# Optimization experiments

Measured on AMD Instinct MI355X. Metric: run time of the kernel, lower is better.

Reference implementation:

```python
import jax, jax.numpy as jnp
import numpy as np

S, B, C, H, W = 5, 2, 128, 24, 24
N_ITER = 3
BN_EPS = 1e-5


def conv2d(x, w, b, pad):
    # x: (N, Cin, H, W), w: (Cout, Cin, kh, kw)
    y = jax.lax.conv_general_dilated(
        x, w, (1, 1), [(pad, pad), (pad, pad)],
        dimension_numbers=('NCHW', 'OIHW', 'NCHW'))
    return y + b[None, :, None, None]


def setup_inputs() -> dict:
    key = jax.random.key(0)
    ks = jax.random.split(key, 8)
    sc = 0.03  # keep pre-softmax logits in a sane range
    d = {}
    d['x'] = jax.random.normal(ks[0], (S, B, C, H, W), jnp.float32) * 0.5
    d['Wf_w'] = jax.random.normal(ks[1], (C, C, 3, 3), jnp.float32) * sc
    d['Wf_b'] = jnp.zeros((C,), jnp.float32)
    d['Wh_w'] = jax.random.normal(ks[2], (C, C, 3, 3), jnp.float32) * sc
    d['Wh_b'] = jnp.zeros((C,), jnp.float32)
    d['Wl_w'] = jax.random.normal(ks[3], (C, C, 3, 3), jnp.float32) * sc
    d['Wl_b'] = jnp.zeros((C,), jnp.float32)
    d['alpha'] = jnp.ones((1,), jnp.float32)
    d['Wc'] = jax.random.normal(ks[4], (C, C), jnp.float32) * sc
    d['Wg_w'] = jax.random.normal(ks[5], (C, C, 3, 3), jnp.float32) * sc
    d['Wg_b'] = jnp.zeros((C,), jnp.float32)
    d['bn_gamma'] = jnp.ones((C,), jnp.float32)
    d['bn_beta'] = jnp.zeros((C,), jnp.float32)
    d['gru_zr_w'] = jax.random.normal(ks[6], (2 * C, 2 * C, 5, 5), jnp.float32) * sc
    d['gru_zr_b'] = jnp.zeros((2 * C,), jnp.float32)
    d['gru_h_w'] = jax.random.normal(ks[7], (C, 2 * C, 5, 5), jnp.float32) * sc
    d['gru_h_b'] = jnp.zeros((C,), jnp.float32)
    d['intra_w'] = jnp.full((1,), 0.5, jnp.float32)
    d['inter_w'] = jnp.full((1,), 0.5, jnp.float32)
    return d


def reference(x, Wf_w, Wf_b, Wh_w, Wh_b, Wl_w, Wl_b, alpha, Wc, Wg_w, Wg_b,
              bn_gamma, bn_beta, gru_zr_w, gru_zr_b, gru_h_w, gru_h_b,
              intra_w, inter_w):
    S_, B_, C_, H_, W_ = x.shape
    N = H_ * W_
    # BatchNorm2d in inference mode with fresh running stats (mean=0, var=1)
    bn_scale = bn_gamma / jnp.sqrt(1.0 + BN_EPS)
    mask = (1.0 - jnp.eye(S_, dtype=x.dtype))[:, :, None, None, None, None]
    h = x
    for _ in range(N_ITER):
        hb = h.reshape(S_ * B_, C_, H_, W_)
        # ---- intra-node self-attention (per node in sequence) ----
        ft = conv2d(hb, Wf_w, Wf_b, 1).reshape(S_, B_, C_, N)
        ht = conv2d(hb, Wh_w, Wh_b, 1).reshape(S_, B_, C_, N)
        lt = conv2d(hb, Wl_w, Wl_b, 1).reshape(S_, B_, C_, N)
        att = jax.nn.softmax(jnp.einsum('sbcn,sbcm->sbnm', ft, ht), axis=-1)
        ctx = jnp.einsum('sbnm,sbcm->sbcn', att, lt).reshape(S_, B_, C_, H_, W_)
        eii = alpha[0] * ctx + h
        # ---- inter-node pairwise attention messages (all i,j pairs) ----
        hf = h.reshape(S_, B_, C_, N)
        yt = jnp.einsum('cd,jbdn->jbcn', Wc, hf)
        eij = jnp.einsum('ibcn,jbcm->ijbnm', hf, yt)  # (S,S,B,N,N)
        eijn = jax.nn.softmax(eij, axis=-1)
        mji = jnp.einsum('ijbnm,jbcm->ijbcn', eijn, hf)  # (S,S,B,C,N)
        m4 = mji.reshape(S_ * S_ * B_, C_, H_, W_)
        g = jax.nn.sigmoid(jnp.mean(conv2d(m4, Wg_w, Wg_b, 1),
                                    axis=(2, 3), keepdims=True))
        mg = (g * m4) * bn_scale[None, :, None, None] + bn_beta[None, :, None, None]
        mg = mg.reshape(S_, S_, B_, C_, H_, W_)
        inter = jnp.sum(mg * mask, axis=1)  # exclude j == i
        msg = intra_w[0] * eii + inter_w[0] * inter
        # ---- ConvGRU update + residual ----
        xi = msg.reshape(S_ * B_, C_, H_, W_)
        zr = jax.nn.sigmoid(conv2d(jnp.concatenate([xi, hb], axis=1),
                                   gru_zr_w, gru_zr_b, 2))
        z, r = zr[:, :C_], zr[:, C_:]
        h_hat = jnp.tanh(conv2d(jnp.concatenate([xi, r * hb], axis=1),
                                gru_h_w, gru_h_b, 2))
        h_new = (1.0 - z) * hb + z * h_hat
        h = (h_new + hb).reshape(S_, B_, C_, H_, W_)
    return h
```

## Files before the change

### kernel.cpp

```cpp
#include <hip/hip_runtime.h>
#include <math.h>

#define S_  5
#define B_  2
#define C_  128
#define N_  576
#define SB  10
#define NPAIR 40
#define C2  256

typedef short v8s __attribute__((ext_vector_type(8)));
typedef float v4f __attribute__((ext_vector_type(4)));

#define GLOBAL_AS __attribute__((address_space(1)))
#define LDS_AS    __attribute__((address_space(3)))

__device__ __forceinline__ unsigned short f2bf(float f) {
    union { float f; unsigned u; } v; v.f = f;
    unsigned r = (v.u + 0x7FFF + ((v.u >> 16) & 1)) >> 16;
    return (unsigned short)r;
}
__device__ __forceinline__ float bf2f(unsigned short h) {
    union { unsigned u; float f; } v; v.u = ((unsigned)h) << 16;
    return v.f;
}

__device__ __forceinline__ void packA5_body(int idx, const float* __restrict__ w,
                                            unsigned short* __restrict__ Apk, int M)
{
    if (idx >= M * 6400) return;
    int r = idx;
    int j = r & 7;      r >>= 3;
    int quad = r & 3;   r >>= 2;
    int l15 = r & 15;   r >>= 4;
    int c = r & 3;      r >>= 2;
    int tap_l = r % 5;  r /= 5;
    int g = r % 5;      r /= 5;
    int ch = r & 1;     r >>= 1;
    int kk = r & 3;     r >>= 2;
    int cgb = r;
    int co = cgb * 64 + c * 16 + l15;
    int ci = kk * 64 + ch * 32 + quad * 8 + j;
    int tap = g * 5 + tap_l;
    Apk[idx] = f2bf(w[((size_t)co * 256 + ci) * 25 + tap]);
}
__device__ __forceinline__ void packA3_body(int idx, const float* __restrict__ wf,
                                            const float* __restrict__ wh,
                                            const float* __restrict__ wl,
                                            unsigned short* __restrict__ Apk)
{
    if (idx >= 384 * 1152) return;
    int r = idx;
    int j = r & 7;      r >>= 3;
    int quad = r & 3;   r >>= 2;
    int l15 = r & 15;   r >>= 4;
    int c = r & 3;      r >>= 2;
    int tap_l = r % 3;  r /= 3;
    int g = r % 3;      r /= 3;
    int ch = r & 1;     r >>= 1;
    int kk = r & 1;     r >>= 1;
    int cgb = r;
    int co = cgb * 64 + c * 16 + l15;
    const float* w = (co < 128) ? wf : (co < 256) ? wh : wl;
    int cl = co & 127;
    int ci = kk * 64 + ch * 32 + quad * 8 + j;
    int tap = g * 3 + tap_l;
    Apk[idx] = f2bf(w[((size_t)cl * 128 + ci) * 9 + tap]);
}
__device__ __forceinline__ void packWc_body(int idx, const float* __restrict__ w,
                                            unsigned short* __restrict__ o)
{
    if (idx < 128 * 128) o[idx] = f2bf(w[idx]);
}
__device__ __forceinline__ void packWgT_body(int idx, const float* __restrict__ w,
                                             float* __restrict__ o)
{
    if (idx >= 128 * 1152) return;
    int co = idx & 127, i = idx >> 7;
    o[(size_t)i * 128 + co] = w[(size_t)co * 1152 + i];
}

__device__ __forceinline__ void tc_body(
    int px0, int img,
    const float* __restrict__ src, const float* __restrict__ zrp,
    const float* __restrict__ zrb,
    unsigned short* __restrict__ dst, unsigned short* __restrict__ vfd)
{
    const size_t PLANE = (size_t)SB * C2 * N_;
    __shared__ float tile[128][9];
    int t = threadIdx.x;
    #pragma unroll
    for (int i = 0; i < 4; ++i) {
        int e = i * 256 + t; int ci = e >> 3; int px = e & 7;
        float v = src[((size_t)img * 128 + ci) * 576 + px0 + px];
        if (zrp) {
            size_t zi = ((size_t)img * C2 + 128 + ci) * 576 + px0 + px;
            float a = zrb[128 + ci];
            #pragma unroll
            for (int k = 0; k < 4; ++k) a += zrp[k * PLANE + zi];
            v *= 1.f / (1.f + __expf(-a));
        }
        tile[ci][px] = v;
        if (vfd) {
            int m = px0 + px;
            int ctile = ci >> 4, l15v = ci & 15;
            int sIdx = m >> 5, quadv = (m >> 3) & 3, j = m & 7;
            vfd[(((size_t)img * 8 + ctile) * 18 + sIdx) * 512 + (quadv * 16 + l15v) * 8 + j] = f2bf(v);
        }
    }
    __syncthreads();
    #pragma unroll
    for (int i = 0; i < 4; ++i) {
        int e = i * 256 + t; int pxl = e >> 7; int ci = e & 127;
        dst[((size_t)img * 576 + px0 + pxl) * 128 + ci] = f2bf(tile[ci][pxl]);
    }
}

__global__ __launch_bounds__(256) void tc_kernel(
    const float* __restrict__ src, const float* __restrict__ zrp,
    const float* __restrict__ zrb,
    unsigned short* __restrict__ dst, unsigned short* __restrict__ vfd)
{
    tc_body(blockIdx.x * 8, blockIdx.y, src, zrp, zrb, dst, vfd);
}

#define NB_A3   1728
#define NB_A5ZR 6400
#define NB_A5H  3200
#define NB_WC   64
#define NB_WGT  576
#define NB_TC   720
__global__ __launch_bounds__(256) void pack_all_kernel(
    const float* __restrict__ Wf_w, const float* __restrict__ Wh_w,
    const float* __restrict__ Wl_w, unsigned short* __restrict__ Wp3,
    const float* __restrict__ zr_w, unsigned short* __restrict__ Wpzr,
    const float* __restrict__ gh_w, unsigned short* __restrict__ Wph,
    const float* __restrict__ Wc,  unsigned short* __restrict__ Wcb,
    const float* __restrict__ Wg_w, float* __restrict__ WgT,
    const float* __restrict__ x, unsigned short* __restrict__ hT16,
    unsigned short* __restrict__ VFi)
{
    int bid = blockIdx.x, t = threadIdx.x;
    if (bid < NB_A3) {
        packA3_body(bid * 256 + t, Wf_w, Wh_w, Wl_w, Wp3);
    } else if (bid < NB_A3 + NB_A5ZR) {
        packA5_body((bid - NB_A3) * 256 + t, zr_w, Wpzr, 256);
    } else if (bid < NB_A3 + NB_A5ZR + NB_A5H) {
        packA5_body((bid - NB_A3 - NB_A5ZR) * 256 + t, gh_w, Wph, 128);
    } else if (bid < NB_A3 + NB_A5ZR + NB_A5H + NB_WC) {
        packWc_body((bid - NB_A3 - NB_A5ZR - NB_A5H) * 256 + t, Wc, Wcb);
    } else if (bid < NB_A3 + NB_A5ZR + NB_A5H + NB_WC + NB_WGT) {
        packWgT_body((bid - NB_A3 - NB_A5ZR - NB_A5H - NB_WC) * 256 + t, Wg_w, WgT);
    } else {
        int b2 = bid - (NB_A3 + NB_A5ZR + NB_A5H + NB_WC + NB_WGT);
        tc_body((b2 % 72) * 8, b2 / 72, x, nullptr, nullptr, hT16, VFi);
    }
}

template<int KD, int R, int CINT, int SPLITK, int MODE>
__device__ __forceinline__ void conv_body(
    int bx, int by, int bz,
    const unsigned short* __restrict__ srcA, const unsigned short* __restrict__ srcB,
    const unsigned short* __restrict__ Apk, int COUT, float* __restrict__ po,
    const float* __restrict__ b0, const float* __restrict__ b1, const float* __restrict__ b2,
    unsigned short* __restrict__ t0, unsigned short* __restrict__ t1,
    unsigned short* __restrict__ t2)
{
    constexpr int PART   = CINT / SPLITK;
    constexpr int NCH    = PART / 32;
    constexpr int NSUB   = NCH * KD;
    constexpr int WR     = 8 + 2 * R;
    constexpr int WC     = 24 + 2 * R;
    constexpr int NPOS   = WR * WC;
    constexpr int NSLOTB = NPOS * 4;
    constexpr int RB     = (NSLOTB + 255) / 256;
    constexpr int AUNITS = KD * 4 * 64;
    constexpr int AR     = AUNITS / 256;
    __shared__ __align__(16) unsigned short Ab[2][AUNITS * 8];
    __shared__ __align__(16) unsigned short Bb[NPOS * 32];

    int f   = bx;
    int kk  = f % SPLITK;
    int cgb = f / SPLITK;
    int pxb = by;
    int img = bz;
    int t = threadIdx.x;
    int wave = t >> 6, lane = t & 63;
    int quad = lane >> 4, l15 = lane & 15;
    int r0 = pxb * 8;

    const int cibase = kk * PART;
    const unsigned short* src = (cibase >= 128) ? srcB : srcA;
    const int cioff0 = cibase & 127;
    const unsigned short* srcI = src + (size_t)img * 576 * 128;

    int posBase[3], pxs[3];
    #pragma unroll
    for (int s = 0; s < 3; ++s) {
        int px = pxb * 192 + wave * 48 + s * 16 + l15;
        pxs[s] = px;
        int pr = px / 24, pc = px % 24;
        posBase[s] = (pr - r0 + R) * WC + pc + R;
    }

    int goffB[RB]; bool gokB[RB];
    #pragma unroll
    for (int rr = 0; rr < RB; ++rr) {
        int idx = rr * 256 + wave * 64 + lane;
        int pos = idx >> 2, slotq = idx & 3;
        int gr = slotq ^ ((pos >> 1) & 3);
        int wr = pos / WC, wc = pos % WC;
        int grow = r0 - R + wr, gcol = wc - R;
        gokB[rr] = (idx < NSLOTB) && grow >= 0 && grow < 24 && gcol >= 0 && gcol < 24;
        goffB[rr] = (grow * 24 + gcol) * 128 + gr * 8;
    }

    auto stageB = [&](int ch) {
        const unsigned short* sp = srcI + cioff0 + ch * 32;
        #pragma unroll
        for (int rr = 0; rr < RB; ++rr) {
            if (gokB[rr]) {
                __builtin_amdgcn_global_load_lds(
                    (const GLOBAL_AS void*)(sp + goffB[rr]),
                    (LDS_AS void*)((char*)&Bb[0] + (size_t)(rr * 256 + wave * 64) * 16),
                    16, 0, 0);
            }
        }
    };
    auto stageA = [&](int sub, int buf) {
        const unsigned short* sp = Apk + ((size_t)((cgb * SPLITK + kk) * NSUB + sub)) * (AUNITS * 8);
        #pragma unroll
        for (int r = 0; r < AR; ++r) {
            int u0 = r * 256 + wave * 64;
            __builtin_amdgcn_global_load_lds(
                (const GLOBAL_AS void*)(sp + (size_t)(u0 + lane) * 8),
                (LDS_AS void*)((char*)&Ab[buf][0] + (size_t)u0 * 16),
                16, 0, 0);
        }
    };

    v4f acc[4][3];
    #pragma unroll
    for (int c = 0; c < 4; ++c)
        #pragma unroll
        for (int s = 0; s < 3; ++s)
            #pragma unroll
            for (int r = 0; r < 4; ++r) acc[c][s][r] = 0.f;

    {
        v8s zv;
        #pragma unroll
        for (int j = 0; j < 8; ++j) zv[j] = 0;
        for (int i = t; i < NPOS * 4; i += 256) ((v8s*)Bb)[i] = zv;
    }
    __syncthreads();
    stageB(0);
    stageA(0, 0);
    __syncthreads();

    int sub = 0;
    #pragma unroll 1
    for (int ch = 0; ch < NCH; ++ch) {
        #pragma unroll 1
        for (int g = 0; g < KD; ++g) {
            if (sub + 1 < NSUB) stageA(sub + 1, (sub + 1) & 1);
            const unsigned short* Ap = &Ab[sub & 1][0];
            #pragma unroll
            for (int tl = 0; tl < KD; ++tl) {
                int doff = (g - R) * WC + (tl - R);
                v8s a[4];
                #pragma unroll
                for (int c = 0; c < 4; ++c)
                    a[c] = *(const v8s*)&Ap[((tl * 4 + c) * 64 + l15 * 4 + quad) * 8];
                v8s b[3];
                #pragma unroll
                for (int s = 0; s < 3; ++s) {
                    int pos = posBase[s] + doff;
                    b[s] = *(const v8s*)&Bb[pos * 32 + ((quad ^ ((pos >> 1) & 3)) << 3)];
                }
                #pragma unroll
                for (int c = 0; c < 4; ++c)
                    #pragma unroll
                    for (int s = 0; s < 3; ++s)
                        acc[c][s] = __builtin_amdgcn_mfma_f32_16x16x32_bf16(a[c], b[s], acc[c][s], 0, 0, 0);
            }
            __syncthreads();
            ++sub;
        }
        if (ch + 1 < NCH) { stageB(ch + 1); __syncthreads(); }
    }

    if (MODE == 0) {
        float* out = po + (size_t)kk * ((size_t)SB * COUT * 576)
                   + ((size_t)img * COUT + cgb * 64) * 576;
        #pragma unroll
        for (int c = 0; c < 4; ++c)
            #pragma unroll
            for (int s = 0; s < 3; ++s)
                #pragma unroll
                for (int r = 0; r < 4; ++r) {
                    int col = c * 16 + quad * 4 + r;
                    out[(size_t)col * 576 + pxs[s]] = acc[c][s][r];
                }
    } else {
        #pragma unroll
        for (int c = 0; c < 4; ++c)
            #pragma unroll
            for (int s = 0; s < 3; ++s) {
                int px = pxs[s];
                #pragma unroll
                for (int r = 0; r < 4; ++r) {
                    int co = cgb * 64 + c * 16 + quad * 4 + r;
                    int which = co >> 7, cl = co & 127;
                    const float* bp = (which == 0) ? b0 : (which == 1) ? b1 : b2;
                    float v = acc[c][s][r] + bp[cl];
                    if (which == 0) {
                        t0[((size_t)img * 576 + px) * 128 + cl] = f2bf(v);
                    } else if (which == 1) {
                        int mt = px >> 4, l15m = px & 15;
                        int kb = cl >> 5, quadk = (cl >> 3) & 3, jj = cl & 7;
                        t1[(((size_t)img * 36 + mt) * 4 + kb) * 512 + (quadk * 16 + l15m) * 8 + jj] = f2bf(v);
                    } else {
                        int ctile = cl >> 4, l15v = cl & 15;
                        int sIdx = px >> 5, quadv = (px >> 3) & 3, jj = px & 7;
                        t2[(((size_t)img * 8 + ctile) * 18 + sIdx) * 512 + (quadv * 16 + l15v) * 8 + jj] = f2bf(v);
                    }
                }
            }
    }
}

template<int KD, int R, int CINT, int SPLITK, int MODE>
__global__ __launch_bounds__(256, 1) void conv_mfma(
    const unsigned short* __restrict__ srcA, const unsigned short* __restrict__ srcB,
    const unsigned short* __restrict__ Apk, int COUT, float* __restrict__ po,
    const float* __restrict__ b0, const float* __restrict__ b1, const float* __restrict__ b2,
    unsigned short* __restrict__ t0, unsigned short* __restrict__ t1,
    unsigned short* __restrict__ t2)
{
    conv_body<KD, R, CINT, SPLITK, MODE>(blockIdx.x, blockIdx.y, blockIdx.z,
        srcA, srcB, Apk, COUT, po, b0, b1, b2, t0, t1, t2);
}

__device__ __forceinline__ void yt_body(
    int mt, int img,
    const unsigned short* __restrict__ hT, const unsigned short* __restrict__ Wcb,
    unsigned short* __restrict__ KFi)
{
    int t = threadIdx.x, wave = t >> 6, lane = t & 63;
    int q = lane >> 4, l15 = lane & 15;
    int n0 = mt * 16;
    v4f acc[2];
    #pragma unroll
    for (int ct = 0; ct < 2; ++ct)
        #pragma unroll
        for (int r = 0; r < 4; ++r) acc[ct][r] = 0.f;
    #pragma unroll
    for (int kk = 0; kk < 4; ++kk) {
        v8s b = *(const v8s*)(hT + ((size_t)img * 576 + n0 + l15) * 128 + kk * 32 + q * 8);
        #pragma unroll
        for (int ct = 0; ct < 2; ++ct) {
            v8s a = *(const v8s*)(Wcb + (size_t)((wave * 2 + ct) * 16 + l15) * 128 + kk * 32 + q * 8);
            acc[ct] = __builtin_amdgcn_mfma_f32_16x16x32_bf16(a, b, acc[ct], 0, 0, 0);
        }
    }
    #pragma unroll
    for (int ct = 0; ct < 2; ++ct) {
        #pragma unroll
        for (int r = 0; r < 4; ++r) {
            int co = (wave * 2 + ct) * 16 + q * 4 + r;
            int kk = co >> 5, quadk = (co >> 3) & 3, j = co & 7;
            KFi[(((size_t)img * 36 + mt) * 4 + kk) * 512 + (quadk * 16 + l15) * 8 + j]
                = f2bf(acc[ct][r]);
        }
    }
}

__global__ __launch_bounds__(256, 1) void conv3_yt_kernel(
    const unsigned short* __restrict__ hT, const unsigned short* __restrict__ Wp3,
    const float* __restrict__ Wf_b, const float* __restrict__ Wh_b,
    const float* __restrict__ Wl_b,
    unsigned short* __restrict__ ftT, unsigned short* __restrict__ KFa,
    unsigned short* __restrict__ VFa,
    const unsigned short* __restrict__ Wcb, unsigned short* __restrict__ KFi)
{
    int bid = blockIdx.x;
    if (bid < 180) {
        conv_body<3, 1, 128, 1, 1>(bid % 6, (bid / 6) % 3, bid / 18,
            hT, hT, Wp3, 384, nullptr, Wf_b, Wh_b, Wl_b, ftT, KFa, VFa);
    } else {
        int b2 = bid - 180;
        yt_body(b2 % 36, b2 / 36, hT, Wcb, KFi);
    }
}

__global__ __launch_bounds__(256) void attn_merged(
    const unsigned short* __restrict__ QTi, const unsigned short* __restrict__ KFa,
    const unsigned short* __restrict__ VFa, float* __restrict__ Of,
    const float* __restrict__ addsrc, const float* __restrict__ alpha,
    const unsigned short* __restrict__ QTe, const unsigned short* __restrict__ KFe,
    const unsigned short* __restrict__ VFe, unsigned short* __restrict__ Oh,
    float* __restrict__ wpart)
{
    __shared__ __align__(16) unsigned short P[32 * 576];
    __shared__ float redmx[4][32];
    __shared__ float redsm[4][32];
    int t = threadIdx.x;
    int wave = t >> 6, lane = t & 63;
    int q = lane >> 4, l15 = lane & 15;

    int bid = blockIdx.x;
    int xcd = bid & 7, slot = bid >> 3;
    int gs = (xcd < 4) ? xcd * 113 + slot : 452 + (xcd - 4) * 112 + slot;
    int p = gs / 18;
    int mt2 = gs - p * 18;
    int n0 = mt2 * 32;

    bool intra = (p < SB);
    int pp = 0;
    const unsigned short *Qp, *Kp, *Vp;
    if (intra) {
        Qp = QTi + ((size_t)p * 576 + n0) * 128;
        Kp = KFa + (size_t)p * 36 * 4 * 512;
        Vp = VFa + (size_t)p * 8 * 18 * 512;
    } else {
        int pe = p - SB;
        int j = pe >> 3; int t2 = pe & 7;
        int b = t2 & 1;  int ii = t2 >> 1;
        int i = ii + (ii >= j ? 1 : 0);
        int qimg = i * 2 + b, kimg = j * 2 + b;
        pp = (i * 4 + (j - (j > i ? 1 : 0))) * 2 + b;
        Qp = QTe + ((size_t)qimg * 576 + n0) * 128;
        Kp = KFe + (size_t)kimg * 36 * 4 * 512;
        Vp = VFe + (size_t)kimg * 8 * 18 * 512;
    }

    v8s aq[2][4];
    #pragma unroll
    for (int qt = 0; qt < 2; ++qt)
        #pragma unroll
        for (int kk = 0; kk < 4; ++kk)
            aq[qt][kk] = *(const v8s*)(Qp + (size_t)(qt * 16 + l15) * 128 + kk * 32 + q * 8);

    v4f S[2][9];
    #pragma unroll
    for (int qt = 0; qt < 2; ++qt)
        #pragma unroll
        for (int i = 0; i < 9; ++i)
            #pragma unroll
            for (int r = 0; r < 4; ++r) S[qt][i][r] = 0.f;

    #pragma unroll
    for (int i = 0; i < 9; ++i) {
        int mtk = wave * 9 + i;
        #pragma unroll
        for (int kk = 0; kk < 4; ++kk) {
            v8s b = *(const v8s*)(Kp + ((size_t)(mtk * 4 + kk)) * 512 + lane * 8);
            S[0][i] = __builtin_amdgcn_mfma_f32_16x16x32_bf16(aq[0][kk], b, S[0][i], 0, 0, 0);
            S[1][i] = __builtin_amdgcn_mfma_f32_16x16x32_bf16(aq[1][kk], b, S[1][i], 0, 0, 0);
        }
    }

    #pragma unroll
    for (int qt = 0; qt < 2; ++qt) {
        #pragma unroll
        for (int r = 0; r < 4; ++r) {
            float m = S[qt][0][r];
            #pragma unroll
            for (int i = 1; i < 9; ++i) m = fmaxf(m, S[qt][i][r]);
            #pragma unroll
            for (int off = 1; off < 16; off <<= 1) m = fmaxf(m, __shfl_xor(m, off));
            if (l15 == 0) redmx[wave][qt * 16 + q * 4 + r] = m;
        }
    }
    __syncthreads();
    float sum[2][4];
    #pragma unroll
    for (int qt = 0; qt < 2; ++qt) {
        #pragma unroll
        for (int r = 0; r < 4; ++r) {
            int rr = qt * 16 + q * 4 + r;
            float g = fmaxf(fmaxf(redmx[0][rr], redmx[1][rr]),
                            fmaxf(redmx[2][rr], redmx[3][rr]));
            float s = 0.f;
            #pragma unroll
            for (int i = 0; i < 9; ++i) { float e = __expf(S[qt][i][r] - g); S[qt][i][r] = e; s += e; }
            #pragma unroll
            for (int off = 1; off < 16; off <<= 1) s += __shfl_xor(s, off);
            sum[qt][r] = s;
        }
    }
    if (l15 == 0) {
        #pragma unroll
        for (int qt = 0; qt < 2; ++qt)
            #pragma unroll
            for (int r = 0; r < 4; ++r) redsm[wave][qt * 16 + q * 4 + r] = sum[qt][r];
    }
    #pragma unroll
    for (int qt = 0; qt < 2; ++qt) {
        #pragma unroll
        for (int i = 0; i < 9; ++i) {
            int m = (wave * 9 + i) * 16 + l15;
            int cm = m >> 3, mo = m & 7;
            #pragma unroll
            for (int r = 0; r < 4; ++r) {
                int n = qt * 16 + q * 4 + r;
                P[n * 576 + ((cm ^ (n & 7)) << 3) + mo] = f2bf(S[qt][i][r]);
            }
        }
    }
    __syncthreads();
    float inv[2][4];
    #pragma unroll
    for (int qt = 0; qt < 2; ++qt)
        #pragma unroll
        for (int r = 0; r < 4; ++r) {
            int rr = qt * 16 + q * 4 + r;
            inv[qt][r] = 1.f / (redsm[0][rr] + redsm[1][rr] + redsm[2][rr] + redsm[3][rr]);
        }

    v4f o[2][2];
    #pragma unroll
    for (int qt = 0; qt < 2; ++qt)
        #pragma unroll
        for (int ct = 0; ct < 2; ++ct)
            #pragma unroll
            for (int r = 0; r < 4; ++r) o[qt][ct][r] = 0.f;

    for (int s = 0; s < 18; ++s) {
        int cm = s * 4 + q;
        v8s a0 = *(const v8s*)&P[l15 * 576 + ((cm ^ (l15 & 7)) << 3)];
        v8s a1 = *(const v8s*)&P[(16 + l15) * 576 + ((cm ^ (l15 & 7)) << 3)];
        #pragma unroll
        for (int ct = 0; ct < 2; ++ct) {
            int ctile = wave * 2 + ct;
            v8s b = *(const v8s*)(Vp + ((size_t)(ctile * 18 + s)) * 512 + lane * 8);
            o[0][ct] = __builtin_amdgcn_mfma_f32_16x16x32_bf16(a0, b, o[0][ct], 0, 0, 0);
            o[1][ct] = __builtin_amdgcn_mfma_f32_16x16x32_bf16(a1, b, o[1][ct], 0, 0, 0);
        }
    }

    if (intra) {
        float al = alpha[0];
        #pragma unroll
        for (int qt = 0; qt < 2; ++qt)
            #pragma unroll
            for (int ct = 0; ct < 2; ++ct) {
                int c = (wave * 2 + ct) * 16 + l15;
                size_t base = ((size_t)p * 128 + c) * 576 + n0 + qt * 16 + q * 4;
                #pragma unroll
                for (int r = 0; r < 4; ++r)
                    Of[base + r] = al * o[qt][ct][r] * inv[qt][r] + addsrc[base + r];
            }
    } else {
        #pragma unroll
        for (int ct = 0; ct < 2; ++ct) {
            int c = (wave * 2 + ct) * 16 + l15;
            float sums[9];
            #pragma unroll
            for (int k = 0; k < 9; ++k) sums[k] = 0.f;
            #pragma unroll
            for (int qt = 0; qt < 2; ++qt) {
                size_t base = ((size_t)pp * 128 + c) * 576 + n0 + qt * 16 + q * 4;
                #pragma unroll
                for (int r = 0; r < 4; ++r) {
                    unsigned short hb = f2bf(o[qt][ct][r] * inv[qt][r]);
                    Oh[base + r] = hb;
                    float v = bf2f(hb);
                    int px = n0 + qt * 16 + q * 4 + r;
                    int row = px / 24, col = px % 24;
                    sums[0] += v;
                    if (row == 0)  sums[1] += v;
                    if (row == 23) sums[2] += v;
                    if (col == 0)  sums[3] += v;
                    if (col == 23) sums[4] += v;
                    if (px == 0)   sums[5] += v;
                    if (px == 23)  sums[6] += v;
                    if (px == 552) sums[7] += v;
                    if (px == 575) sums[8] += v;
                }
            }
            #pragma unroll
            for (int k = 0; k < 9; ++k) {
                sums[k] += __shfl_xor(sums[k], 16);
                sums[k] += __shfl_xor(sums[k], 32);
            }
            if (q == 0) {
                float* wp = wpart + (((size_t)pp * 18 + mt2) * 9) * 128 + c;
                #pragma unroll
                for (int k = 0; k < 9; ++k) wp[k * 128] = sums[k];
            }
        }
    }
}

__global__ __launch_bounds__(256) void g_kernel(
    const float* __restrict__ wpart, const float* __restrict__ WgT,
    const float* __restrict__ Wgb, float* __restrict__ g)
{
    __shared__ float sw[C_ * 9];
    __shared__ float acc2[256];
    int pair = blockIdx.x; int t = threadIdx.x;
    int co = t & 127, half = t >> 7;
    const float* base = wpart + (size_t)pair * 18 * 9 * 128 + co;
    float raw[9];
    #pragma unroll
    for (int k = 0; k < 9; ++k) raw[k] = 0.f;
    for (int mt = half; mt < 18; mt += 2) {
        #pragma unroll
        for (int k = 0; k < 9; ++k) raw[k] += base[(mt * 9 + k) * 128];
    }
    if (half == 1) {
        #pragma unroll
        for (int k = 0; k < 9; ++k) sw[co * 9 + k] = raw[k];
    }
    __syncthreads();
    if (half == 0) {
        #pragma unroll
        for (int k = 0; k < 9; ++k) raw[k] += sw[co * 9 + k];
        float rowsub[3] = {raw[2], 0.f, raw[1]};
        float colsub[3] = {raw[4], 0.f, raw[3]};
        float corner[9] = {raw[8], 0.f, raw[7], 0.f, 0.f, 0.f, raw[6], 0.f, raw[5]};
        #pragma unroll
        for (int ky = 0; ky < 3; ++ky)
            #pragma unroll
            for (int kx = 0; kx < 3; ++kx)
                sw[co * 9 + ky * 3 + kx] = raw[0] - rowsub[ky] - colsub[kx] + corner[ky * 3 + kx];
    }
    __syncthreads();
    float acc = 0.f;
    const float* wg = WgT + (size_t)half * 576 * 128 + co;
    const float* swh = sw + half * 576;
    for (int i = 0; i < 576; ++i) acc += wg[(size_t)i * 128] * swh[i];
    acc2[t] = acc;
    __syncthreads();
    if (half == 0) {
        float m = (acc + acc2[t + 128]) * (1.f / 576.f) + Wgb[co];
        g[pair * C_ + co] = 1.f / (1.f + __expf(-m));
    }
}

__global__ __launch_bounds__(256) void msg_tc_kernel(
    const float* __restrict__ eii, const unsigned short* __restrict__ mji,
    const float* __restrict__ g, const float* __restrict__ bn_gamma,
    const float* __restrict__ bn_beta, const float* __restrict__ intra_w,
    const float* __restrict__ inter_w, unsigned short* __restrict__ msgT)
{
    __shared__ float tile[128][9];
    int img = blockIdx.y, px0 = blockIdx.x * 8, t = threadIdx.x;
    int s = img >> 1, b = img & 1;
    float iw = intra_w[0], ew = inter_w[0];
    #pragma unroll
    for (int i = 0; i < 4; ++i) {
        int e = i * 256 + t; int ci = e >> 3; int pxl = e & 7;
        int px = px0 + pxl;
        float scale = bn_gamma[ci] * rsqrtf(1.f + 1e-5f);
        float acc = 0.f;
        #pragma unroll
        for (int jj = 0; jj < 4; ++jj) {
            int pidx = (s * 4 + jj) * 2 + b;
            acc += g[pidx * C_ + ci] * bf2f(mji[((size_t)pidx * C_ + ci) * N_ + px]);
        }
        float inter = scale * acc + 4.f * bn_beta[ci];
        tile[ci][pxl] = iw * eii[((size_t)img * C_ + ci) * N_ + px] + ew * inter;
    }
    __syncthreads();
    #pragma unroll
    for (int i = 0; i < 4; ++i) {
        int e = i * 256 + t; int pxl = e >> 7; int ci = e & 127;
        msgT[((size_t)img * 576 + px0 + pxl) * 128 + ci] = f2bf(tile[ci][pxl]);
    }
}

__global__ __launch_bounds__(256) void update_tc_kernel(
    const float* __restrict__ zrp, const float* __restrict__ zrb,
    const float* __restrict__ hhp, const float* __restrict__ ghb,
    const float* __restrict__ h, float* __restrict__ out,
    unsigned short* __restrict__ hTn, unsigned short* __restrict__ VFn, int last)
{
    const size_t ZP = (size_t)SB * C2 * N_;
    const size_t HP = (size_t)SB * C_ * N_;
    __shared__ float tile[128][9];
    int img = blockIdx.y, px0 = blockIdx.x * 8, t = threadIdx.x;
    #pragma unroll
    for (int i = 0; i < 4; ++i) {
        int e = i * 256 + t; int ci = e >> 3; int pxl = e & 7;
        int px = px0 + pxl;
        size_t zi = ((size_t)img * C2 + ci) * N_ + px;
        float za = zrb[ci];
        #pragma unroll
        for (int k = 0; k < 4; ++k) za += zrp[k * ZP + zi];
        float z = 1.f / (1.f + __expf(-za));
        size_t hi = ((size_t)img * C_ + ci) * N_ + px;
        float ha = ghb[ci];
        #pragma unroll
        for (int k = 0; k < 4; ++k) ha += hhp[k * HP + hi];
        float hh = tanhf(ha);
        float o = (2.f - z) * h[hi] + z * hh;
        out[hi] = o;
        tile[ci][pxl] = o;
        if (!last) {
            int ctile = ci >> 4, l15v = ci & 15;
            int sIdx = px >> 5, quadv = (px >> 3) & 3, j = px & 7;
            VFn[(((size_t)img * 8 + ctile) * 18 + sIdx) * 512 + (quadv * 16 + l15v) * 8 + j] = f2bf(o);
        }
    }
    if (!last) {
        __syncthreads();
        #pragma unroll
        for (int i = 0; i < 4; ++i) {
            int e = i * 256 + t; int pxl = e >> 7; int ci = e & 127;
            hTn[((size_t)img * 576 + px0 + pxl) * 128 + ci] = f2bf(tile[ci][pxl]);
        }
    }
}

extern "C" void kernel_launch(void* const* d_in, const int* in_sizes, int n_in,
                              void* d_out, int out_size, void* d_ws, size_t ws_size,
                              hipStream_t stream)
{
    const float* x      = (const float*)d_in[0];
    const float* Wf_w   = (const float*)d_in[1];
    const float* Wf_b   = (const float*)d_in[2];
    const float* Wh_w   = (const float*)d_in[3];
    const float* Wh_b   = (const float*)d_in[4];
    const float* Wl_w   = (const float*)d_in[5];
    const float* Wl_b   = (const float*)d_in[6];
    const float* alpha  = (const float*)d_in[7];
    const float* Wc     = (const float*)d_in[8];
    const float* Wg_w   = (const float*)d_in[9];
    const float* Wg_b   = (const float*)d_in[10];
    const float* bng    = (const float*)d_in[11];
    const float* bnb    = (const float*)d_in[12];
    const float* zr_w   = (const float*)d_in[13];
    const float* zr_b   = (const float*)d_in[14];
    const float* gh_w   = (const float*)d_in[15];
    const float* gh_b   = (const float*)d_in[16];
    const float* intraw = (const float*)d_in[17];
    const float* interw = (const float*)d_in[18];
    float* outp = (float*)d_out;

    float* f = (float*)d_ws;
    const size_t SZ = (size_t)SB * C_ * N_;
    float* hbuf  = f; f += SZ;
    float* eii   = f; f += SZ;
    float* zrp   = f; f += 4 * (size_t)SB * C2 * N_;
    float* hhp   = f; f += 4 * SZ;
    float* wpart = f; f += (size_t)NPAIR * 18 * 9 * 128;
    float* gbuf  = f; f += (size_t)NPAIR * C_;
    float* WgT   = f; f += (size_t)128 * 1152;
    unsigned short* us = (unsigned short*)f;
    unsigned short* mji16  = us; us += (size_t)NPAIR * C_ * N_;
    unsigned short* hT16   = us; us += SZ;
    unsigned short* hc16   = us; us += SZ;
    unsigned short* msgT16 = us; us += SZ;
    unsigned short* ftT    = us; us += SZ;
    unsigned short* KFa    = us; us += SZ;
    unsigned short* VFa    = us; us += SZ;
    unsigned short* Wp3    = us; us += (size_t)384 * 1152;
    unsigned short* Wpzr   = us; us += (size_t)256 * 6400;
    unsigned short* Wph    = us; us += (size_t)128 * 6400;
    unsigned short* Wcb    = us; us += (size_t)128 * 128;
    unsigned short* KFi    = us; us += SZ;

    unsigned short* VFi    = hc16;
    unsigned short* rhbT16 = hc16;

    pack_all_kernel<<<NB_A3 + NB_A5ZR + NB_A5H + NB_WC + NB_WGT + NB_TC, 256, 0, stream>>>(
        Wf_w, Wh_w, Wl_w, Wp3, zr_w, Wpzr, gh_w, Wph, Wc, Wcb, Wg_w, WgT,
        x, hT16, VFi);

    const float* hcur = x;
    for (int it = 0; it < 3; ++it) {
        float* hout = (it == 2) ? outp : hbuf;

        conv3_yt_kernel<<<540, 256, 0, stream>>>(
            hT16, Wp3, Wf_b, Wh_b, Wl_b, ftT, KFa, VFa, Wcb, KFi);
        attn_merged<<<900, 256, 0, stream>>>(
            ftT, KFa, VFa, eii, hcur, alpha, hT16, KFi, VFi, mji16, wpart);
        g_kernel<<<NPAIR, 256, 0, stream>>>(wpart, WgT, Wg_b, gbuf);
        msg_tc_kernel<<<dim3(72, SB), 256, 0, stream>>>(
            eii, mji16, gbuf, bng, bnb, intraw, interw, msgT16);
        conv_mfma<5, 2, 256, 4, 0><<<dim3(16, 3, SB), 256, 0, stream>>>(
            msgT16, hT16, Wpzr, 256, zrp, nullptr, nullptr, nullptr, nullptr, nullptr, nullptr);
        tc_kernel<<<dim3(72, SB), 256, 0, stream>>>(hcur, zrp, zr_b, rhbT16, nullptr);
        conv_mfma<5, 2, 256, 4, 0><<<dim3(8, 3, SB), 256, 0, stream>>>(
            msgT16, rhbT16, Wph, 128, hhp, nullptr, nullptr, nullptr, nullptr, nullptr, nullptr);
        update_tc_kernel<<<dim3(72, SB), 256, 0, stream>>>(
            zrp, zr_b, hhp, gh_b, hcur, hout, hT16, VFi, (it == 2) ? 1 : 0);
        hcur = hout;
    }
}
```

Before: 520.0 us.

## Move r-independent half of GRU candidate conv into the zr conv launch

The candidate-state conv is split along its K dimension. The split-K slices that read only the message channels are computed in the same launch as the z/r gate conv, and only the slices that need r*h run after the gate kernel. This shortens the serial chain between the gate conv and the update kernel and fills the first launch with more blocks. The cost is a larger first launch, which may add a partial wave, and it relies on split indices 0-1 covering the message half of the input channels.

```diff
diff --git a/kernel.cpp b/kernel.cpp
--- a/kernel.cpp
+++ b/kernel.cpp
@@ -330,16 +330,31 @@
     }
 }
 
-template<int KD, int R, int CINT, int SPLITK, int MODE>
-__global__ __launch_bounds__(256, 1) void conv_mfma(
-    const unsigned short* __restrict__ srcA, const unsigned short* __restrict__ srcB,
-    const unsigned short* __restrict__ Apk, int COUT, float* __restrict__ po,
-    const float* __restrict__ b0, const float* __restrict__ b1, const float* __restrict__ b2,
-    unsigned short* __restrict__ t0, unsigned short* __restrict__ t1,
-    unsigned short* __restrict__ t2)
-{
-    conv_body<KD, R, CINT, SPLITK, MODE>(blockIdx.x, blockIdx.y, blockIdx.z,
-        srcA, srcB, Apk, COUT, po, b0, b1, b2, t0, t1, t2);
+__global__ __launch_bounds__(256, 1) void conv_zr_hA_kernel(
+    const unsigned short* __restrict__ msgT, const unsigned short* __restrict__ hT,
+    const unsigned short* __restrict__ Wpzr, float* __restrict__ zrp,
+    const unsigned short* __restrict__ Wph, float* __restrict__ hhp)
+{
+    int bx = blockIdx.x;
+    if (bx < 16) {
+        conv_body<5, 2, 256, 4, 0>(bx, blockIdx.y, blockIdx.z,
+            msgT, hT, Wpzr, 256, zrp, nullptr, nullptr, nullptr, nullptr, nullptr, nullptr);
+    } else {
+        int b2 = bx - 16;
+        int bxa = (b2 >> 1) * 4 + (b2 & 1);
+        conv_body<5, 2, 256, 4, 0>(bxa, blockIdx.y, blockIdx.z,
+            msgT, hT, Wph, 128, hhp, nullptr, nullptr, nullptr, nullptr, nullptr, nullptr);
+    }
+}
+
+__global__ __launch_bounds__(256, 1) void conv_hB_kernel(
+    const unsigned short* __restrict__ msgT, const unsigned short* __restrict__ rhbT,
+    const unsigned short* __restrict__ Wph, float* __restrict__ hhp)
+{
+    int b2 = blockIdx.x;
+    int bxa = (b2 >> 1) * 4 + 2 + (b2 & 1);
+    conv_body<5, 2, 256, 4, 0>(bxa, blockIdx.y, blockIdx.z,
+        msgT, rhbT, Wph, 128, hhp, nullptr, nullptr, nullptr, nullptr, nullptr, nullptr);
 }
 
 __device__ __forceinline__ void yt_body(
@@ -781,11 +796,11 @@
         g_kernel<<<NPAIR, 256, 0, stream>>>(wpart, WgT, Wg_b, gbuf);
         msg_tc_kernel<<<dim3(72, SB), 256, 0, stream>>>(
             eii, mji16, gbuf, bng, bnb, intraw, interw, msgT16);
-        conv_mfma<5, 2, 256, 4, 0><<<dim3(16, 3, SB), 256, 0, stream>>>(
-            msgT16, hT16, Wpzr, 256, zrp, nullptr, nullptr, nullptr, nullptr, nullptr, nullptr);
+        conv_zr_hA_kernel<<<dim3(20, 3, SB), 256, 0, stream>>>(
+            msgT16, hT16, Wpzr, zrp, Wph, hhp);
         tc_kernel<<<dim3(72, SB), 256, 0, stream>>>(hcur, zrp, zr_b, rhbT16, nullptr);
-        conv_mfma<5, 2, 256, 4, 0><<<dim3(8, 3, SB), 256, 0, stream>>>(
-            msgT16, rhbT16, Wph, 128, hhp, nullptr, nullptr, nullptr, nullptr, nullptr, nullptr);
+        conv_hB_kernel<<<dim3(4, 3, SB), 256, 0, stream>>>(
+            msgT16, rhbT16, Wph, hhp);
         update_tc_kernel<<<dim3(72, SB), 256, 0, stream>>>(
             zrp, zr_b, hhp, gh_b, hcur, hout, hT16, VFi, (it == 2) ? 1 : 0);
         hcur = hout;
```

Result: slower. 555.1 us (+6.8%).
